# Optimization experiments

Measured on AMD Instinct MI355X. Metric: run time of the kernel, lower is better.

## Reference

```python
import jax, jax.numpy as jnp
import numpy as np

SQ, SK, D = 8192, 8192, 128

def setup_inputs() -> dict:
    k = jax.random.key(0)
    kq, kk, kv = jax.random.split(k, 3)
    query = jax.random.normal(kq, (SQ, D), dtype=jnp.float32)
    key = jax.random.normal(kk, (SK, D), dtype=jnp.float32)
    value = jax.random.normal(kv, (SK, D), dtype=jnp.float32)
    return {"query": query, "key": key, "value": value}

def reference(query, key, value):
    # attn_weights = dot_general(q, k, contract last dims) -> [Sq, Sk]
    attn_weights = jnp.einsum('qd,kd->qk', query, key)
    # softmax over key dims (second half of attn_weights dims)
    attn_weights = jax.nn.softmax(attn_weights, axis=-1)
    # dropout is identity: train=False -> deterministic
    # y = dot_general(attn_weights, value, contract key dims) -> [Sq, Dv]
    y = jnp.einsum('qk,kd->qd', attn_weights, value)
    return y
```

## Files before the change

kernel.cpp:

```cpp
#include <hip/hip_runtime.h>
#include <hip/hip_bf16.h>
#include <stdint.h>

#define SQ 8192
#define SK 8192
#define DH 128
#define L2E 1.4426950408889634f
#define CB 40.0f

typedef __attribute__((ext_vector_type(8))) _Float16 f16x8;
typedef __attribute__((ext_vector_type(8))) short bf16x8;
typedef __attribute__((ext_vector_type(16))) float f32x16;
typedef __attribute__((ext_vector_type(4))) short s16x4;
typedef __attribute__((ext_vector_type(4))) unsigned int u32x4;

__device__ __forceinline__ short f2h(float f) {
  _Float16 h = (_Float16)f;
  return __builtin_bit_cast(short, h);
}
__device__ __forceinline__ short f2bf(float f) {
  uint32_t u = __builtin_bit_cast(uint32_t, f);
  u = (u + 0x7FFFu + ((u >> 16) & 1u)) >> 16;
  return (short)u;
}

__device__ __forceinline__ void gl_lds16(const void* g, void* l) {
  __builtin_amdgcn_global_load_lds(
      (const __attribute__((address_space(1))) void*)g,
      (__attribute__((address_space(3))) void*)l, 16, 0, 0);
}

__global__ __launch_bounds__(256) void prep_kernel(const float* __restrict__ K,
                                                   const float* __restrict__ V,
                                                   short* __restrict__ Kimg,
                                                   short* __restrict__ Vimg) {
  __shared__ short T[32][136];
  const int tid = threadIdx.x;
  if (blockIdx.x < 256) {
    const int kb = blockIdx.x;
#pragma unroll
    for (int i = 0; i < 4; ++i) {
      int fi = i * 256 + tid;
      int key = fi >> 5;
      int dc = (fi & 31) * 4;
      float4 v = ((const float4*)K)[(size_t)(kb * 32 + key) * (DH / 4) + (fi & 31)];
      T[key][dc + 0] = f2h(v.x); T[key][dc + 1] = f2h(v.y);
      T[key][dc + 2] = f2h(v.z); T[key][dc + 3] = f2h(v.w);
    }
    __syncthreads();
#pragma unroll
    for (int i = 0; i < 2; ++i) {
      int ci = i * 256 + tid;
      int kc = ci >> 6, lane = ci & 63;
      int row = lane & 31;
      int k0 = kc * 16 + (lane >> 5) * 8;
      s16x4 o0, o1;
      o0.x = T[row][k0 + 0]; o0.y = T[row][k0 + 1];
      o0.z = T[row][k0 + 2]; o0.w = T[row][k0 + 3];
      o1.x = T[row][k0 + 4]; o1.y = T[row][k0 + 5];
      o1.z = T[row][k0 + 6]; o1.w = T[row][k0 + 7];
      s16x4* dst = (s16x4*)(Kimg + (size_t)kb * 4096 + ci * 8);
      dst[0] = o0; dst[1] = o1;
    }
  } else {
    const int kb = blockIdx.x - 256;
#pragma unroll
    for (int i = 0; i < 4; ++i) {
      int fi = i * 256 + tid;
      int key = fi >> 5;
      int dc = (fi & 31) * 4;
      float4 v = ((const float4*)V)[(size_t)(kb * 32 + key) * (DH / 4) + (fi & 31)];
      T[key][dc + 0] = f2bf(v.x); T[key][dc + 1] = f2bf(v.y);
      T[key][dc + 2] = f2bf(v.z); T[key][dc + 3] = f2bf(v.w);
    }
    __syncthreads();
#pragma unroll
    for (int i = 0; i < 2; ++i) {
      int ci = i * 256 + tid;
      int lane = ci & 63;
      int g = ci >> 6;
      int dt = g & 3, ks = g >> 2;
      int base = ks * 16 + (lane >> 5) * 4;
      int d = dt * 32 + (lane & 31);
      s16x4 o0, o1;
      o0.x = T[base + 0][d]; o0.y = T[base + 1][d];
      o0.z = T[base + 2][d]; o0.w = T[base + 3][d];
      o1.x = T[base + 8][d]; o1.y = T[base + 9][d];
      o1.z = T[base + 10][d]; o1.w = T[base + 11][d];
      s16x4* dst = (s16x4*)(Vimg + (size_t)kb * 4096 + ci * 8);
      dst[0] = o0; dst[1] = o1;
    }
  }
}

#define NITD 32
__global__ __launch_bounds__(512, 2) void attn_q128d(const float* __restrict__ Q,
                                                     const short* __restrict__ Kimg,
                                                     const short* __restrict__ Vimg,
                                                     float* __restrict__ Opart,
                                                     float* __restrict__ lpart) {
  __shared__ __align__(16) char smem[67584];
  const int tid = threadIdx.x;
  const int w = tid >> 6;
  const int lane = tid & 63;
  const int half = lane >> 5;
  const int l32 = lane & 31;
  const int qh = w >> 1;
  const int kw = w & 1;
  const int b = blockIdx.x;
  const int kh = (b >> 1) & 3;
  const int qb = ((b >> 3) << 1) | (b & 1);
  const int qrow0 = qb * 128 + qh * 32;
  const int kb0 = kh * 64;

  f16x8 qf[8];
  {
    const float* qp = Q + (size_t)(qrow0 + l32) * DH + half * 8;
#pragma unroll
    for (int kc = 0; kc < 8; ++kc) {
      float4 a = *(const float4*)(qp + kc * 16);
      float4 b2 = *(const float4*)(qp + kc * 16 + 4);
      f16x8 h;
      h[0] = (_Float16)a.x; h[1] = (_Float16)a.y; h[2] = (_Float16)a.z; h[3] = (_Float16)a.w;
      h[4] = (_Float16)b2.x; h[5] = (_Float16)b2.y; h[6] = (_Float16)b2.z; h[7] = (_Float16)b2.w;
      qf[kc] = h;
    }
  }

  f32x16 of[4];
#pragma unroll
  for (int dt = 0; dt < 4; ++dt)
#pragma unroll
    for (int c = 0; c < 16; ++c) of[dt][c] = 0.f;
  float l_lane = 0.f;

  for (int i = 0; i < w; ++i) __builtin_amdgcn_s_sleep(8);

  f16x8 kf[8];
  bf16x8 vf[8];
  {
    const short* kp = Kimg + (size_t)(kb0 + kw) * 4096;
    const short* vp = Vimg + (size_t)(kb0 + kw) * 4096;
#pragma unroll
    for (int kc = 0; kc < 8; ++kc) kf[kc] = *(const f16x8*)(kp + kc * 512 + lane * 8);
#pragma unroll
    for (int g = 0; g < 8; ++g) vf[g] = *(const bf16x8*)(vp + g * 512 + lane * 8);
  }

  for (int t = 0; t < NITD; ++t) {
    f32x16 sacc;
#pragma unroll
    for (int c = 0; c < 16; ++c) sacc[c] = 0.f;
    __builtin_amdgcn_s_setprio(1);
#pragma unroll
    for (int kc = 0; kc < 8; ++kc)
      sacc = __builtin_amdgcn_mfma_f32_32x32x16_f16(kf[kc], qf[kc], sacc, 0, 0, 0);
    __builtin_amdgcn_s_setprio(0);

    if (t + 1 < NITD) {
      const short* kp = Kimg + (size_t)(kb0 + (t + 1) * 2 + kw) * 4096;
#pragma unroll
      for (int kc = 0; kc < 8; ++kc) kf[kc] = *(const f16x8*)(kp + kc * 512 + lane * 8);
    }

    u32x4 pav0, pav1;
#pragma unroll
    for (int r = 0; r < 4; ++r) {
      float pA = __builtin_amdgcn_exp2f(fmaf(sacc[2 * r], L2E, -CB));
      float pB = __builtin_amdgcn_exp2f(fmaf(sacc[2 * r + 1], L2E, -CB));
      float pC = __builtin_amdgcn_exp2f(fmaf(sacc[8 + 2 * r], L2E, -CB));
      float pD = __builtin_amdgcn_exp2f(fmaf(sacc[8 + 2 * r + 1], L2E, -CB));
      l_lane += (pA + pB) + (pC + pD);
      uint32_t uA = __builtin_bit_cast(uint32_t, pA); uA += 0x7FFFu + ((uA >> 16) & 1u);
      uint32_t uB = __builtin_bit_cast(uint32_t, pB); uB += 0x7FFFu + ((uB >> 16) & 1u);
      uint32_t uC = __builtin_bit_cast(uint32_t, pC); uC += 0x7FFFu + ((uC >> 16) & 1u);
      uint32_t uD = __builtin_bit_cast(uint32_t, pD); uD += 0x7FFFu + ((uD >> 16) & 1u);
      pav0[r] = __builtin_amdgcn_perm(uB, uA, 0x07060302u);
      pav1[r] = __builtin_amdgcn_perm(uD, uC, 0x07060302u);
    }
    bf16x8 pa0 = __builtin_bit_cast(bf16x8, pav0);
    bf16x8 pa1 = __builtin_bit_cast(bf16x8, pav1);

    __builtin_amdgcn_s_setprio(1);
#pragma unroll
    for (int dt = 0; dt < 4; ++dt) {
      of[dt] = __builtin_amdgcn_mfma_f32_32x32x16_bf16(pa0, vf[dt], of[dt], 0, 0, 0);
      of[dt] = __builtin_amdgcn_mfma_f32_32x32x16_bf16(pa1, vf[4 + dt], of[dt], 0, 0, 0);
    }
    __builtin_amdgcn_s_setprio(0);

    if (t + 1 < NITD) {
      const short* vp = Vimg + (size_t)(kb0 + (t + 1) * 2 + kw) * 4096;
#pragma unroll
      for (int g = 0; g < 8; ++g) vf[g] = *(const bf16x8*)(vp + g * 512 + lane * 8);
    }
  }

  float l_tot = l_lane + __shfl_xor(l_lane, 32);

  __syncthreads();
  float* mO = (float*)smem;
  float* R = mO + qh * 4224;
  if (kw == 0) {
#pragma unroll
    for (int c = 0; c < 16; ++c) {
      const int row = (c & 3) + 8 * (c >> 2) + 4 * half;
      float* br = R + row * 132;
#pragma unroll
      for (int dt = 0; dt < 4; ++dt) br[dt * 32 + l32] = of[dt][c];
    }
    if (half == 0) R[l32 * 132 + 128] = l_tot;
  }
  __syncthreads();
  if (kw == 1) {
#pragma unroll
    for (int c = 0; c < 16; ++c) {
      const int row = (c & 3) + 8 * (c >> 2) + 4 * half;
      float* br = R + row * 132;
#pragma unroll
      for (int dt = 0; dt < 4; ++dt) br[dt * 32 + l32] += of[dt][c];
    }
    if (half == 0) R[l32 * 132 + 128] += l_tot;
  }
  __syncthreads();
  {
    const int row = tid >> 2;
    const int cg = tid & 3;
    const float* p = mO + (row >> 5) * 4224 + (row & 31) * 132;
    float* dst = Opart + ((size_t)kh << 20) + (size_t)(qb * 128 + row) * DH + cg * 32;
#pragma unroll
    for (int k = 0; k < 8; ++k)
      ((float4*)dst)[k] = ((const float4*)(p + cg * 32))[k];
    if (cg == 0) lpart[kh * SQ + qb * 128 + row] = p[128];
  }
}

__global__ __launch_bounds__(256) void combine4(const float* __restrict__ Opart,
                                                const float* __restrict__ lpart,
                                                float* __restrict__ out) {
  const int idx = blockIdx.x * 256 + threadIdx.x;
  const int row = idx >> 5;
  const int c4 = (idx & 31) * 4;
  const float inv = 1.f / (lpart[row] + lpart[SQ + row] +
                           lpart[2 * SQ + row] + lpart[3 * SQ + row]);
  const size_t off = (size_t)row * DH + c4;
  float4 a = *(const float4*)(Opart + off);
  const float4 b = *(const float4*)(Opart + (1u << 20) + off);
  const float4 c = *(const float4*)(Opart + (2u << 20) + off);
  const float4 d = *(const float4*)(Opart + (3u << 20) + off);
  a.x = (a.x + b.x + c.x + d.x) * inv;
  a.y = (a.y + b.y + c.y + d.y) * inv;
  a.z = (a.z + b.z + c.z + d.z) * inv;
  a.w = (a.w + b.w + c.w + d.w) * inv;
  *(float4*)(out + off) = a;
}

__global__ __launch_bounds__(512, 2) void attn_fb(const float* __restrict__ Q,
                                                  const short* __restrict__ Kimg,
                                                  const short* __restrict__ Vimg,
                                                  float* __restrict__ Oa,
                                                  float* __restrict__ Ob,
                                                  float* __restrict__ l0,
                                                  float* __restrict__ l1) {
  __shared__ __align__(16) char smem[131072];
  short* stg = (short*)smem;
  const int tid = threadIdx.x;
  const int w = tid >> 6;
  const int lane = tid & 63;
  const int half = lane >> 5;
  const int l32 = lane & 31;
  const int qh = w >> 2;
  const int ks = w & 3;
  const int qb = blockIdx.x >> 1;
  const int kh = blockIdx.x & 1;
  const int qrow0 = qb * 64 + qh * 32;
  const int kb0 = kh * 128;

  f16x8 qf[8];
  {
    const float* qp = Q + (size_t)(qrow0 + l32) * DH + half * 8;
#pragma unroll
    for (int kc = 0; kc < 8; ++kc) {
      float4 a = *(const float4*)(qp + kc * 16);
      float4 b = *(const float4*)(qp + kc * 16 + 4);
      f16x8 h;
      h[0] = (_Float16)a.x; h[1] = (_Float16)a.y; h[2] = (_Float16)a.z; h[3] = (_Float16)a.w;
      h[4] = (_Float16)b.x; h[5] = (_Float16)b.y; h[6] = (_Float16)b.z; h[7] = (_Float16)b.w;
      qf[kc] = h;
    }
  }

  f32x16 of[4];
#pragma unroll
  for (int dt = 0; dt < 4; ++dt)
#pragma unroll
    for (int c = 0; c < 16; ++c) of[dt][c] = 0.f;
  float l_lane = 0.f;

  const short* gsrc = (w < 4 ? Kimg : Vimg) + ((size_t)kb0 + ks) * 4096 + lane * 8;
  short* lbase = stg + ((w >= 4) ? 16384 : 0) + ks * 4096;

  auto STAGE = [&](int c, int t) {
    const short* g = gsrc + (size_t)t * 4 * 4096;
    short* l = lbase + c * 32768;
#pragma unroll
    for (int j = 0; j < 8; ++j)
      gl_lds16(g + j * 512, l + j * 512);
  };

  STAGE(0, 0);
  __syncthreads();
  int cur = 0;

  for (int t = 0; t < 32; ++t) {
    const short* bk = stg + cur * 32768 + ks * 4096 + lane * 8;
    f16x8 kf[8];
#pragma unroll
    for (int kc = 0; kc < 8; ++kc) kf[kc] = *(const f16x8*)(bk + kc * 512);

    if (t + 1 < 32) STAGE(cur ^ 1, t + 1);

    f32x16 sacc;
#pragma unroll
    for (int c = 0; c < 16; ++c) sacc[c] = 0.f;
#pragma unroll
    for (int kc = 0; kc < 8; ++kc)
      sacc = __builtin_amdgcn_mfma_f32_32x32x16_f16(kf[kc], qf[kc], sacc, 0, 0, 0);

    const short* bv = stg + cur * 32768 + 16384 + ks * 4096 + lane * 8;
    bf16x8 vf[8];
#pragma unroll
    for (int g2 = 0; g2 < 8; ++g2) vf[g2] = *(const bf16x8*)(bv + g2 * 512);

    u32x4 pav0, pav1;
#pragma unroll
    for (int r = 0; r < 4; ++r) {
      float pA = __builtin_amdgcn_exp2f(fmaf(sacc[2 * r], L2E, -CB));
      float pB = __builtin_amdgcn_exp2f(fmaf(sacc[2 * r + 1], L2E, -CB));
      float pC = __builtin_amdgcn_exp2f(fmaf(sacc[8 + 2 * r], L2E, -CB));
      float pD = __builtin_amdgcn_exp2f(fmaf(sacc[8 + 2 * r + 1], L2E, -CB));
      l_lane += (pA + pB) + (pC + pD);
      uint32_t uA = __builtin_bit_cast(uint32_t, pA); uA += 0x7FFFu + ((uA >> 16) & 1u);
      uint32_t uB = __builtin_bit_cast(uint32_t, pB); uB += 0x7FFFu + ((uB >> 16) & 1u);
      uint32_t uC = __builtin_bit_cast(uint32_t, pC); uC += 0x7FFFu + ((uC >> 16) & 1u);
      uint32_t uD = __builtin_bit_cast(uint32_t, pD); uD += 0x7FFFu + ((uD >> 16) & 1u);
      pav0[r] = __builtin_amdgcn_perm(uB, uA, 0x07060302u);
      pav1[r] = __builtin_amdgcn_perm(uD, uC, 0x07060302u);
    }
    bf16x8 pa0 = __builtin_bit_cast(bf16x8, pav0);
    bf16x8 pa1 = __builtin_bit_cast(bf16x8, pav1);

#pragma unroll
    for (int dt = 0; dt < 4; ++dt) {
      of[dt] = __builtin_amdgcn_mfma_f32_32x32x16_bf16(pa0, vf[dt], of[dt], 0, 0, 0);
      of[dt] = __builtin_amdgcn_mfma_f32_32x32x16_bf16(pa1, vf[4 + dt], of[dt], 0, 0, 0);
    }

    __syncthreads();
    cur ^= 1;
  }

  float l_tot = l_lane + __shfl_xor(l_lane, 32);

  __syncthreads();
  float* mO = (float*)smem;
  float* R = mO + (qh * 2 + (ks & 1)) * 4224;
  if (ks < 2) {
#pragma unroll
    for (int c = 0; c < 16; ++c) {
      const int row = (c & 3) + 8 * (c >> 2) + 4 * half;
      float* br = R + row * 132;
#pragma unroll
      for (int dt = 0; dt < 4; ++dt) br[dt * 32 + l32] = of[dt][c];
    }
    if (half == 0) R[l32 * 132 + 128] = l_tot;
  }
  __syncthreads();
  if (ks >= 2) {
#pragma unroll
    for (int c = 0; c < 16; ++c) {
      const int row = (c & 3) + 8 * (c >> 2) + 4 * half;
      float* br = R + row * 132;
#pragma unroll
      for (int dt = 0; dt < 4; ++dt) br[dt * 32 + l32] += of[dt][c];
    }
    if (half == 0) R[l32 * 132 + 128] += l_tot;
  }
  __syncthreads();
  {
    const int row = tid >> 3;
    const int cg = tid & 7;
    const int qh2 = row >> 5;
    const int r32 = row & 31;
    const float* Ra = mO + (qh2 * 2 + 0) * 4224 + r32 * 132;
    const float* Rb = mO + (qh2 * 2 + 1) * 4224 + r32 * 132;
    float lp = Ra[128] + Rb[128];
    float* dst = (kh ? Ob : Oa) + (size_t)(qb * 64 + row) * DH + cg * 16;
#pragma unroll
    for (int k = 0; k < 4; ++k) {
      float4 a = *(const float4*)(Ra + cg * 16 + k * 4);
      float4 b = *(const float4*)(Rb + cg * 16 + k * 4);
      a.x += b.x; a.y += b.y; a.z += b.z; a.w += b.w;
      *(float4*)(dst + k * 4) = a;
    }
    if (cg == 0) (kh ? l1 : l0)[qb * 64 + row] = lp;
  }
}

__global__ __launch_bounds__(256) void combine2(float* __restrict__ Oa,
                                                const float* __restrict__ Ob,
                                                const float* __restrict__ l0,
                                                const float* __restrict__ l1) {
  const int idx = blockIdx.x * 256 + threadIdx.x;
  const int row = idx >> 5;
  const int c4 = (idx & 31) * 4;
  const float inv = 1.f / (l0[row] + l1[row]);
  float* pa = Oa + (size_t)row * DH + c4;
  const float* pb = Ob + (size_t)row * DH + c4;
  float4 a = *(const float4*)pa;
  float4 b = *(const float4*)pb;
  a.x = (a.x + b.x) * inv; a.y = (a.y + b.y) * inv;
  a.z = (a.z + b.z) * inv; a.w = (a.w + b.w) * inv;
  *(float4*)pa = a;
}

extern "C" void kernel_launch(void* const* d_in, const int* in_sizes, int n_in,
                              void* d_out, int out_size, void* d_ws, size_t ws_size,
                              hipStream_t stream) {
  const float* Q = (const float*)d_in[0];
  const float* K = (const float*)d_in[1];
  const float* V = (const float*)d_in[2];
  float* out = (float*)d_out;
  char* ws = (char*)d_ws;
  short* Kimg = (short*)ws;
  short* Vimg = (short*)(ws + 2097152);
  prep_kernel<<<512, 256, 0, stream>>>(K, V, Kimg, Vimg);
  if (ws_size >= (size_t)21102592) {
    float* Opart = (float*)(ws + 4194304);
    float* lpart = (float*)(ws + 20971520);
    attn_q128d<<<256, 512, 0, stream>>>(Q, Kimg, Vimg, Opart, lpart);
    combine4<<<SQ * DH / 4 / 256, 256, 0, stream>>>(Opart, lpart, out);
  } else {
    float* Ob = (float*)(ws + 4194304);
    float* l0 = (float*)(ws + 8388608);
    float* l1 = l0 + SQ;
    attn_fb<<<SQ / 64 * 2, 512, 0, stream>>>(Q, Kimg, Vimg, out, Ob, l0, l1);
    combine2<<<SQ * DH / 4 / 256, 256, 0, stream>>>(out, Ob, l0, l1);
  }
}
```

Baseline: 121.0 us.

## Split attention into 32-row query blocks with four key-split waves per block

Replaces the 128-query-row, 512-thread attention kernel with a 32-query-row, 256-thread kernel launched over 1024 blocks. Each of the four waves now handles an interleaved quarter of the key chunks within a key split and runs half as many iterations. The explicit software prefetch of K/V fragments, staggered wave sleeps and setprio hints are removed, and loads are now issued inside the loop just before use. The LDS reduction now merges four waves, two at a time. The aim is more blocks and higher occupancy to hide latency, at the cost of losing explicit load/compute overlap and re-reading K/V across more blocks.

```diff
diff --git a/kernel.cpp b/kernel.cpp
--- a/kernel.cpp
+++ b/kernel.cpp
@@ -93,24 +93,22 @@
   }
 }
 
-#define NITD 32
-__global__ __launch_bounds__(512, 2) void attn_q128d(const float* __restrict__ Q,
+#define NITQ 16
+__global__ __launch_bounds__(256, 3) void attn_q32x4(const float* __restrict__ Q,
                                                      const short* __restrict__ Kimg,
                                                      const short* __restrict__ Vimg,
                                                      float* __restrict__ Opart,
                                                      float* __restrict__ lpart) {
-  __shared__ __align__(16) char smem[67584];
+  __shared__ __align__(16) float mO[2 * 4224];
   const int tid = threadIdx.x;
   const int w = tid >> 6;
   const int lane = tid & 63;
   const int half = lane >> 5;
   const int l32 = lane & 31;
-  const int qh = w >> 1;
-  const int kw = w & 1;
   const int b = blockIdx.x;
-  const int kh = (b >> 1) & 3;
-  const int qb = ((b >> 3) << 1) | (b & 1);
-  const int qrow0 = qb * 128 + qh * 32;
+  const int kh = b & 3;
+  const int qb = b >> 2;
+  const int qrow0 = qb * 32;
   const int kb0 = kh * 64;
 
   f16x8 qf[8];
@@ -134,34 +132,24 @@
     for (int c = 0; c < 16; ++c) of[dt][c] = 0.f;
   float l_lane = 0.f;
 
-  for (int i = 0; i < w; ++i) __builtin_amdgcn_s_sleep(8);
-
-  f16x8 kf[8];
-  bf16x8 vf[8];
-  {
-    const short* kp = Kimg + (size_t)(kb0 + kw) * 4096;
-    const short* vp = Vimg + (size_t)(kb0 + kw) * 4096;
-#pragma unroll
-    for (int kc = 0; kc < 8; ++kc) kf[kc] = *(const f16x8*)(kp + kc * 512 + lane * 8);
-#pragma unroll
-    for (int g = 0; g < 8; ++g) vf[g] = *(const bf16x8*)(vp + g * 512 + lane * 8);
-  }
-
-  for (int t = 0; t < NITD; ++t) {
+  const short* kp = Kimg + (size_t)(kb0 + w) * 4096 + lane * 8;
+  const short* vp = Vimg + (size_t)(kb0 + w) * 4096 + lane * 8;
+
+  for (int t = 0; t < NITQ; ++t) {
+    f16x8 kf[8];
+#pragma unroll
+    for (int kc = 0; kc < 8; ++kc) kf[kc] = *(const f16x8*)(kp + kc * 512);
+
     f32x16 sacc;
 #pragma unroll
     for (int c = 0; c < 16; ++c) sacc[c] = 0.f;
-    __builtin_amdgcn_s_setprio(1);
 #pragma unroll
     for (int kc = 0; kc < 8; ++kc)
       sacc = __builtin_amdgcn_mfma_f32_32x32x16_f16(kf[kc], qf[kc], sacc, 0, 0, 0);
-    __builtin_amdgcn_s_setprio(0);
-
-    if (t + 1 < NITD) {
-      const short* kp = Kimg + (size_t)(kb0 + (t + 1) * 2 + kw) * 4096;
-#pragma unroll
-      for (int kc = 0; kc < 8; ++kc) kf[kc] = *(const f16x8*)(kp + kc * 512 + lane * 8);
-    }
+
+    bf16x8 vf[8];
+#pragma unroll
+    for (int g2 = 0; g2 < 8; ++g2) vf[g2] = *(const bf16x8*)(vp + g2 * 512);
 
     u32x4 pav0, pav1;
 #pragma unroll
@@ -181,27 +169,21 @@
     bf16x8 pa0 = __builtin_bit_cast(bf16x8, pav0);
     bf16x8 pa1 = __builtin_bit_cast(bf16x8, pav1);
 
-    __builtin_amdgcn_s_setprio(1);
 #pragma unroll
     for (int dt = 0; dt < 4; ++dt) {
       of[dt] = __builtin_amdgcn_mfma_f32_32x32x16_bf16(pa0, vf[dt], of[dt], 0, 0, 0);
       of[dt] = __builtin_amdgcn_mfma_f32_32x32x16_bf16(pa1, vf[4 + dt], of[dt], 0, 0, 0);
     }
-    __builtin_amdgcn_s_setprio(0);
-
-    if (t + 1 < NITD) {
-      const short* vp = Vimg + (size_t)(kb0 + (t + 1) * 2 + kw) * 4096;
-#pragma unroll
-      for (int g = 0; g < 8; ++g) vf[g] = *(const bf16x8*)(vp + g * 512 + lane * 8);
-    }
+
+    kp += 4 * 4096;
+    vp += 4 * 4096;
   }
 
   float l_tot = l_lane + __shfl_xor(l_lane, 32);
 
   __syncthreads();
-  float* mO = (float*)smem;
-  float* R = mO + qh * 4224;
-  if (kw == 0) {
+  float* R = mO + (w & 1) * 4224;
+  if (w < 2) {
 #pragma unroll
     for (int c = 0; c < 16; ++c) {
       const int row = (c & 3) + 8 * (c >> 2) + 4 * half;
@@ -212,7 +194,7 @@
     if (half == 0) R[l32 * 132 + 128] = l_tot;
   }
   __syncthreads();
-  if (kw == 1) {
+  if (w >= 2) {
 #pragma unroll
     for (int c = 0; c < 16; ++c) {
       const int row = (c & 3) + 8 * (c >> 2) + 4 * half;
@@ -224,14 +206,20 @@
   }
   __syncthreads();
   {
-    const int row = tid >> 2;
-    const int cg = tid & 3;
-    const float* p = mO + (row >> 5) * 4224 + (row & 31) * 132;
-    float* dst = Opart + ((size_t)kh << 20) + (size_t)(qb * 128 + row) * DH + cg * 32;
-#pragma unroll
-    for (int k = 0; k < 8; ++k)
-      ((float4*)dst)[k] = ((const float4*)(p + cg * 32))[k];
-    if (cg == 0) lpart[kh * SQ + qb * 128 + row] = p[128];
+    const int row = tid >> 3;
+    const int cg = tid & 7;
+    const float* Ra = mO + row * 132 + cg * 16;
+    const float* Rb = mO + 4224 + row * 132 + cg * 16;
+    float lp = mO[row * 132 + 128] + mO[4224 + row * 132 + 128];
+    float* dst = Opart + ((size_t)kh << 20) + (size_t)(qrow0 + row) * DH + cg * 16;
+#pragma unroll
+    for (int k = 0; k < 4; ++k) {
+      float4 a = *(const float4*)(Ra + k * 4);
+      float4 b2 = *(const float4*)(Rb + k * 4);
+      a.x += b2.x; a.y += b2.y; a.z += b2.z; a.w += b2.w;
+      *(float4*)(dst + k * 4) = a;
+    }
+    if (cg == 0) lpart[kh * SQ + qrow0 + row] = lp;
   }
 }
 
@@ -438,7 +426,7 @@
   if (ws_size >= (size_t)21102592) {
     float* Opart = (float*)(ws + 4194304);
     float* lpart = (float*)(ws + 20971520);
-    attn_q128d<<<256, 512, 0, stream>>>(Q, Kimg, Vimg, Opart, lpart);
+    attn_q32x4<<<1024, 256, 0, stream>>>(Q, Kimg, Vimg, Opart, lpart);
     combine4<<<SQ * DH / 4 / 256, 256, 0, stream>>>(Opart, lpart, out);
   } else {
     float* Ob = (float*)(ws + 4194304);
```

Result: slower. 125.8 us (+4.0%).
